# Kernel optimization log

Measured on AMD Instinct MI355X. Metric: run time of the kernel, lower is better.

The kernel has to match this reference:

```python
import jax, jax.numpy as jnp
import numpy as np

HEADS, DEPTH, KS = 4, 16, 3
PAD = KS // 2
LN_EPS = 1e-3   # keras LayerNormalization default
BN_EPS = 1e-3   # keras BatchNormalization default


def _layernorm(x, g, b):
    m = jnp.mean(x, axis=-1, keepdims=True)
    v = jnp.var(x, axis=-1, keepdims=True)
    return (x - m) * jax.lax.rsqrt(v + LN_EPS) * g + b


def setup_inputs() -> dict:
    key = jax.random.key(0)
    ks = jax.random.split(key, 12)
    B, H, W, C, FF = 4, 384, 384, 64, 128
    s = 0.05
    return {
        "x": jax.random.normal(ks[0], (B, H, W, C), jnp.float32),
        "wq": jax.random.normal(ks[1], (C, C), jnp.float32) * s,
        "wk": jax.random.normal(ks[2], (C, C), jnp.float32) * s,
        "wv": jax.random.normal(ks[3], (C, C), jnp.float32) * s,
        "ln1_g": jnp.ones((C,), jnp.float32),
        "ln1_b": jnp.zeros((C,), jnp.float32),
        "ff1_w": jax.random.normal(ks[4], (C, FF), jnp.float32) * s,
        "ff1_b": jnp.zeros((FF,), jnp.float32),
        "ff2_w": jax.random.normal(ks[5], (FF, C), jnp.float32) * s,
        "ff2_b": jnp.zeros((C,), jnp.float32),
        "ln2_g": jnp.ones((C,), jnp.float32),
        "ln2_b": jnp.zeros((C,), jnp.float32),
        "w_fuse": jax.random.normal(ks[6], (C, C), jnp.float32) * s,
        "bn_g": jax.random.uniform(ks[7], (C,), jnp.float32, 0.5, 1.5),
        "bn_b": jax.random.normal(ks[8], (C,), jnp.float32) * s,
        "bn_mean": jax.random.normal(ks[9], (C,), jnp.float32) * s,
        "bn_var": jax.random.uniform(ks[10], (C,), jnp.float32, 0.5, 1.5),
    }


def reference(x, wq, wk, wv, ln1_g, ln1_b, ff1_w, ff1_b, ff2_w, ff2_b,
              ln2_g, ln2_b, w_fuse, bn_g, bn_b, bn_mean, bn_var):
    B, H, W, C = x.shape
    # 1x1-conv projections == per-pixel dense over channels
    q = jnp.einsum('bhwc,cd->bhwd', x, wq).reshape(B, H, W, HEADS, DEPTH)
    k = jnp.einsum('bhwc,cd->bhwd', x, wk)
    v = jnp.einsum('bhwc,cd->bhwd', x, wv)
    # SAME zero-padding, matching tf.image.extract_patches
    kp = jnp.pad(k, ((0, 0), (PAD, PAD), (PAD, PAD), (0, 0)))
    vp = jnp.pad(v, ((0, 0), (PAD, PAD), (PAD, PAD), (0, 0)))
    # scores for each of the ks*ks offsets via shifted slices (no im2col blowup)
    sims = []
    for dy in range(KS):
        for dx in range(KS):
            ksh = kp[:, dy:dy + H, dx:dx + W, :].reshape(B, H, W, HEADS, DEPTH)
            sims.append(jnp.einsum('bhwnd,bhwnd->bhwn', q, ksh))
    sim = jnp.stack(sims, axis=3) / jnp.sqrt(jnp.float32(DEPTH))  # [B,H,W,ka,heads]
    attn = jax.nn.softmax(sim, axis=3)
    out = jnp.zeros_like(q)  # [B,H,W,heads,depth]
    i = 0
    for dy in range(KS):
        for dx in range(KS):
            vsh = vp[:, dy:dy + H, dx:dx + W, :].reshape(B, H, W, HEADS, DEPTH)
            out = out + attn[:, :, :, i, :, None] * vsh
            i += 1
    out = out.reshape(B, H, W, C)
    # residual (res_proj is None since C % heads == 0) + LN
    out = _layernorm(x + out, ln1_g, ln1_b)
    # token FFN with residual + LN
    ff = jax.nn.relu(jnp.einsum('bhwc,cf->bhwf', out, ff1_w) + ff1_b)
    ff = jnp.einsum('bhwf,fc->bhwc', ff, ff2_w) + ff2_b
    out = _layernorm(out + ff, ln2_g, ln2_b)
    # fuse 1x1 conv + BN (inference mode, moving stats) + relu
    out = jnp.einsum('bhwc,cd->bhwd', out, w_fuse)
    scale = bn_g * jax.lax.rsqrt(bn_var + BN_EPS)
    out = out * scale + (bn_b - bn_mean * scale)
    return jax.nn.relu(out)
```

## Files before the change

kernel.cpp:

```cpp
#include <hip/hip_runtime.h>

#define MTOT 589824

typedef __attribute__((ext_vector_type(8))) short bf16x8;
typedef __attribute__((ext_vector_type(4))) float f32x4;
#define MFMA16 __builtin_amdgcn_mfma_f32_16x16x32_bf16

__device__ __forceinline__ unsigned short f2bf(float f) {
    union { float f; unsigned u; } x; x.f = f;
    unsigned r = x.u + 0x7FFFu + ((x.u >> 16) & 1u);
    return (unsigned short)(r >> 16);
}
__device__ __forceinline__ float bf2f(unsigned short h) {
    union { unsigned u; float f; } x; x.u = ((unsigned)h) << 16;
    return x.f;
}
__device__ __forceinline__ float2 bfpair(int v) {
    union { unsigned u; float f; } a, b;
    a.u = ((unsigned)v) << 16;
    b.u = ((unsigned)v) & 0xffff0000u;
    return make_float2(a.f, b.f);
}
__device__ __forceinline__ int is_bf16(const void* ln1g) {
    return ((const unsigned short*)ln1g)[0] != 0;
}
__device__ __forceinline__ float ldp(const void* p, int i, int isbf) {
    return isbf ? bf2f(((const unsigned short*)p)[i]) : ((const float*)p)[i];
}

__global__ void k_prep(const void* wq, const void* wk, const void* wv,
                       const void* ln1g, const void* ln1b,
                       const void* ff1w, const void* ff1b,
                       const void* ff2w, const void* ff2b,
                       const void* ln2g, const void* ln2b,
                       const void* wfuse, const void* bng, const void* bnb,
                       const void* bnm, const void* bnv,
                       unsigned short* Wbase, float* P) {
    const int isbf = is_bf16(ln1g);
    const int tid = blockIdx.x * blockDim.x + threadIdx.x;
    const int stride = gridDim.x * blockDim.x;
    unsigned short* Wqkv = Wbase;
    unsigned short* W1 = Wbase + 12288;
    unsigned short* W2 = W1 + 8192;
    unsigned short* WF = W2 + 8192;
    for (int i = tid; i < 12288; i += stride) {
        int n = i >> 6, k = i & 63;
        float v;
        if (n < 64)        v = ldp(wq, k*64 + n, isbf) * 0.25f;
        else if (n < 128)  v = ldp(wk, k*64 + (n-64), isbf);
        else               v = ldp(wv, k*64 + (n-128), isbf);
        Wqkv[n*64 + k] = f2bf(v);
    }
    for (int i = tid; i < 8192; i += stride) {
        int n = i >> 6, k = i & 63;
        W1[n*64 + k] = f2bf(ldp(ff1w, k*128 + n, isbf));
    }
    for (int i = tid; i < 8192; i += stride) {
        int n = i >> 7, k = i & 127;
        W2[n*128 + k] = f2bf(ldp(ff2w, k*64 + n, isbf));
    }
    for (int i = tid; i < 4096; i += stride) {
        int n = i >> 6, k = i & 63;
        WF[n*64 + k] = f2bf(ldp(wfuse, k*64 + n, isbf));
    }
    for (int i = tid; i < 64; i += stride) {
        P[i]       = ldp(ln1g, i, isbf);
        P[64+i]    = ldp(ln1b, i, isbf);
        P[256+i]   = ldp(ff2b, i, isbf);
        P[320+i]   = ldp(ln2g, i, isbf);
        P[384+i]   = ldp(ln2b, i, isbf);
        float sc   = ldp(bng, i, isbf) * rsqrtf(ldp(bnv, i, isbf) + 1e-3f);
        P[448+i]   = sc;
        P[512+i]   = ldp(bnb, i, isbf) - ldp(bnm, i, isbf) * sc;
    }
    for (int i = tid; i < 128; i += stride) P[128+i] = ldp(ff1b, i, isbf);
}

__device__ __forceinline__ int rowOf(int hy, int hx) {
    if (hy >= 1 && hy <= 8 && hx >= 1 && hx <= 8) return (hy - 1) * 8 + (hx - 1);
    if (hy == 0) return 64 + hx;
    if (hy == 9) return 74 + hx;
    if (hx == 0) return 84 + (hy - 1);
    return 92 + (hy - 1);
}

__global__ __launch_bounds__(256) void k_fused(
    const void* __restrict__ xg, const void* __restrict__ ln1g,
    const unsigned short* __restrict__ Wqkv, const unsigned short* __restrict__ W1,
    const unsigned short* __restrict__ W2, const unsigned short* __restrict__ WF,
    const float* __restrict__ P, void* __restrict__ outg) {
    __shared__ __align__(16) unsigned short xh[112 * 64];
    __shared__ __align__(16) unsigned short kvb[112 * 132];
    __shared__ __align__(16) unsigned short qy[64 * 72];
    const int t = threadIdx.x;
    const int isbf = is_bf16(ln1g);
    const int bid = ((int)blockIdx.x & 7) * 1152 + ((int)blockIdx.x >> 3);
    const int bb = bid / 2304;
    const int tile = bid - bb * 2304;
    const int by = tile / 48, bx = tile - by * 48;
    const long imgbase = (long)bb * 147456;

    if (isbf) {
        const unsigned short* xs = (const unsigned short*)xg;
        for (int i = t; i < 800; i += 256) {
            int p = i >> 3, c8 = i & 7;
            int hy = p / 10, hx = p - hy * 10;
            int r = rowOf(hy, hx);
            int gy = by * 8 + hy - 1, gx = bx * 8 + hx - 1;
            int4 val = {0, 0, 0, 0};
            if ((unsigned)gy < 384u && (unsigned)gx < 384u)
                val = *(const int4*)(xs + (imgbase + (long)gy * 384 + gx) * 64 + c8 * 8);
            *(int4*)&xh[r * 64 + ((c8 ^ (r & 7)) << 3)] = val;
        }
    } else {
        const float* xs = (const float*)xg;
        for (int i = t; i < 1600; i += 256) {
            int p = i >> 4, c4 = i & 15;
            int hy = p / 10, hx = p - hy * 10;
            int r = rowOf(hy, hx);
            int gy = by * 8 + hy - 1, gx = bx * 8 + hx - 1;
            ushort4 hv = {0, 0, 0, 0};
            if ((unsigned)gy < 384u && (unsigned)gx < 384u) {
                float4 f = *(const float4*)(xs + (imgbase + (long)gy * 384 + gx) * 64 + c4 * 4);
                hv.x = f2bf(f.x); hv.y = f2bf(f.y); hv.z = f2bf(f.z); hv.w = f2bf(f.w);
            }
            int c8 = c4 >> 1;
            *(ushort4*)&xh[r * 64 + (((c8 ^ (r & 7)) << 3) | ((c4 & 1) << 2))] = hv;
        }
    }
    if (t < 96) {
        int4 zz = {0, 0, 0, 0};
        *(int4*)&xh[(100 + (t >> 3)) * 64 + ((t & 7) << 3)] = zz;
    }

    float4 rf0, rf1, rf2, rf3; int4 ri0, ri1;
    {
        const int px = t >> 2, qtr = t & 3;
        const long pofs = (imgbase + (long)(by*8 + (px >> 3)) * 384 + bx*8 + (px & 7)) * 64 + qtr * 16;
        if (isbf) {
            const int4* xp = (const int4*)((const unsigned short*)xg + pofs);
            ri0 = xp[0]; ri1 = xp[1];
        } else {
            const float4* xp = (const float4*)((const float*)xg + pofs);
            rf0 = xp[0]; rf1 = xp[1]; rf2 = xp[2]; rf3 = xp[3];
        }
    }
    __syncthreads();

    const int w = t >> 6, l = t & 63, lm = l & 15, q4 = l >> 4;
    #pragma unroll 2
    for (int uu = 0; uu < 14; ++uu) {
        int u = uu * 4 + w;
        int rt = u >> 3, nt = u & 7;
        int row = rt * 16 + lm, sw = row & 7;
        const bf16x8 a0 = *(const bf16x8*)&xh[row * 64 + ((q4 ^ sw) << 3)];
        const bf16x8 a1 = *(const bf16x8*)&xh[row * 64 + (((q4 + 4) ^ sw) << 3)];
        const unsigned short* wp = Wqkv + (64 + nt * 16 + lm) * 64 + q4 * 8;
        bf16x8 b0 = *(const bf16x8*)wp;
        bf16x8 b1 = *(const bf16x8*)(wp + 32);
        f32x4 acc = {0.f, 0.f, 0.f, 0.f};
        acc = MFMA16(a0, b0, acc, 0, 0, 0);
        acc = MFMA16(a1, b1, acc, 0, 0, 0);
        #pragma unroll
        for (int r = 0; r < 4; ++r)
            kvb[(rt * 16 + q4 * 4 + r) * 132 + nt * 16 + lm] = f2bf(acc[r]);
    }
    #pragma unroll
    for (int uu = 0; uu < 4; ++uu) {
        int row = uu * 16 + lm, sw = row & 7;
        const bf16x8 a0 = *(const bf16x8*)&xh[row * 64 + ((q4 ^ sw) << 3)];
        const bf16x8 a1 = *(const bf16x8*)&xh[row * 64 + (((q4 + 4) ^ sw) << 3)];
        const unsigned short* wp = Wqkv + (w * 16 + lm) * 64 + q4 * 8;
        bf16x8 b0 = *(const bf16x8*)wp;
        bf16x8 b1 = *(const bf16x8*)(wp + 32);
        f32x4 acc = {0.f, 0.f, 0.f, 0.f};
        acc = MFMA16(a0, b0, acc, 0, 0, 0);
        acc = MFMA16(a1, b1, acc, 0, 0, 0);
        #pragma unroll
        for (int r = 0; r < 4; ++r)
            qy[(uu * 16 + q4 * 4 + r) * 72 + w * 16 + lm] = f2bf(acc[r]);
    }
    __syncthreads();

    {
        const int h = w, py = l >> 3, px8 = l & 7;
        float qv[16];
        {
            const int4* qp2 = (const int4*)&qy[l * 72 + h * 16];
            int4 qa = qp2[0], qb4 = qp2[1];
            float2 p0;
            p0 = bfpair(qa.x);  qv[0]  = p0.x; qv[1]  = p0.y;
            p0 = bfpair(qa.y);  qv[2]  = p0.x; qv[3]  = p0.y;
            p0 = bfpair(qa.z);  qv[4]  = p0.x; qv[5]  = p0.y;
            p0 = bfpair(qa.w);  qv[6]  = p0.x; qv[7]  = p0.y;
            p0 = bfpair(qb4.x); qv[8]  = p0.x; qv[9]  = p0.y;
            p0 = bfpair(qb4.y); qv[10] = p0.x; qv[11] = p0.y;
            p0 = bfpair(qb4.z); qv[12] = p0.x; qv[13] = p0.y;
            p0 = bfpair(qb4.w); qv[14] = p0.x; qv[15] = p0.y;
        }
        int rn9[9];
        #pragma unroll
        for (int e = 0; e < 9; ++e) {
            int dy = e / 3, dx = e - dy * 3;
            rn9[e] = rowOf(py + dy, px8 + dx);
        }
        float w9[9];
        #pragma unroll
        for (int e = 0; e < 9; ++e) {
            const int2* kp = (const int2*)&kvb[rn9[e] * 132 + h * 16];
            float sacc = 0.f;
            #pragma unroll
            for (int j = 0; j < 4; ++j) {
                int2 kk = kp[j];
                float2 pa = bfpair(kk.x), pb = bfpair(kk.y);
                sacc += qv[j*4+0]*pa.x + qv[j*4+1]*pa.y
                      + qv[j*4+2]*pb.x + qv[j*4+3]*pb.y;
            }
            w9[e] = sacc;
        }
        float mx = w9[0];
        #pragma unroll
        for (int e = 1; e < 9; ++e) mx = fmaxf(mx, w9[e]);
        float den = 0.f;
        #pragma unroll
        for (int e = 0; e < 9; ++e) { w9[e] = __expf(w9[e] - mx); den += w9[e]; }
        const float inv = 1.f / den;
        float att[16];
        #pragma unroll
        for (int i = 0; i < 16; ++i) att[i] = 0.f;
        #pragma unroll
        for (int e = 0; e < 9; ++e) {
            const int2* vp = (const int2*)&kvb[rn9[e] * 132 + 64 + h * 16];
            const float wgt = w9[e] * inv;
            #pragma unroll
            for (int j = 0; j < 4; ++j) {
                int2 vv = vp[j];
                float2 pa = bfpair(vv.x), pb = bfpair(vv.y);
                att[j*4+0] += wgt*pa.x;
                att[j*4+1] += wgt*pa.y;
                att[j*4+2] += wgt*pb.x;
                att[j*4+3] += wgt*pb.y;
            }
        }
        int4 o0, o1;
        o0.x = (int)((unsigned)f2bf(att[0])  | ((unsigned)f2bf(att[1])  << 16));
        o0.y = (int)((unsigned)f2bf(att[2])  | ((unsigned)f2bf(att[3])  << 16));
        o0.z = (int)((unsigned)f2bf(att[4])  | ((unsigned)f2bf(att[5])  << 16));
        o0.w = (int)((unsigned)f2bf(att[6])  | ((unsigned)f2bf(att[7])  << 16));
        o1.x = (int)((unsigned)f2bf(att[8])  | ((unsigned)f2bf(att[9])  << 16));
        o1.y = (int)((unsigned)f2bf(att[10]) | ((unsigned)f2bf(att[11]) << 16));
        o1.z = (int)((unsigned)f2bf(att[12]) | ((unsigned)f2bf(att[13]) << 16));
        o1.w = (int)((unsigned)f2bf(att[14]) | ((unsigned)f2bf(att[15]) << 16));
        *(int4*)&qy[l * 72 + h * 16]     = o0;
        *(int4*)&qy[l * 72 + h * 16 + 8] = o1;
    }
    __syncthreads();

    {
        const int px = t >> 2, qtr = t & 3;
        float v[16];
        const int2* ap = (const int2*)&qy[px * 72 + qtr * 16];
        #pragma unroll
        for (int j = 0; j < 4; ++j) {
            int2 u = ap[j];
            float2 pa = bfpair(u.x), pb = bfpair(u.y);
            v[j*4+0] = pa.x; v[j*4+1] = pa.y; v[j*4+2] = pb.x; v[j*4+3] = pb.y;
        }
        if (isbf) {
            float2 pa = bfpair(ri0.x), pb = bfpair(ri0.y), pc = bfpair(ri0.z), pd = bfpair(ri0.w);
            v[0] += pa.x; v[1] += pa.y; v[2] += pb.x; v[3] += pb.y;
            v[4] += pc.x; v[5] += pc.y; v[6] += pd.x; v[7] += pd.y;
            pa = bfpair(ri1.x); pb = bfpair(ri1.y); pc = bfpair(ri1.z); pd = bfpair(ri1.w);
            v[8]  += pa.x; v[9]  += pa.y; v[10] += pb.x; v[11] += pb.y;
            v[12] += pc.x; v[13] += pc.y; v[14] += pd.x; v[15] += pd.y;
        } else {
            v[0]  += rf0.x; v[1]  += rf0.y; v[2]  += rf0.z; v[3]  += rf0.w;
            v[4]  += rf1.x; v[5]  += rf1.y; v[6]  += rf1.z; v[7]  += rf1.w;
            v[8]  += rf2.x; v[9]  += rf2.y; v[10] += rf2.z; v[11] += rf2.w;
            v[12] += rf3.x; v[13] += rf3.y; v[14] += rf3.z; v[15] += rf3.w;
        }
        float s = 0.f, ss = 0.f;
        #pragma unroll
        for (int c = 0; c < 16; ++c) { s += v[c]; ss += v[c]*v[c]; }
        s  += __shfl_xor(s, 1);  ss += __shfl_xor(ss, 1);
        s  += __shfl_xor(s, 2);  ss += __shfl_xor(ss, 2);
        const float mean = s * (1.f/64.f);
        const float var  = ss * (1.f/64.f) - mean*mean;
        const float rs   = rsqrtf(var + 1e-3f);
        unsigned short* wp2 = &qy[px * 72 + qtr * 16];
        #pragma unroll
        for (int c = 0; c < 16; ++c)
            wp2[c] = f2bf((v[c] - mean)*rs*P[qtr*16 + c] + P[64 + qtr*16 + c]);
    }
    __syncthreads();

    unsigned short* hh = kvb;
    {
        const bf16x8 a0 = *(const bf16x8*)&qy[(w*16 + lm)*72 + q4*8];
        const bf16x8 a1 = *(const bf16x8*)&qy[(w*16 + lm)*72 + 32 + q4*8];
        #pragma unroll
        for (int nt = 0; nt < 8; ++nt) {
            const unsigned short* wp = W1 + (nt*16 + lm)*64 + q4*8;
            bf16x8 b0 = *(const bf16x8*)wp;
            bf16x8 b1 = *(const bf16x8*)(wp + 32);
            f32x4 acc = {0.f, 0.f, 0.f, 0.f};
            acc = MFMA16(a0, b0, acc, 0, 0, 0);
            acc = MFMA16(a1, b1, acc, 0, 0, 0);
            const float bias = P[128 + nt*16 + lm];
            #pragma unroll
            for (int r = 0; r < 4; ++r)
                hh[(w*16 + q4*4 + r)*136 + nt*16 + lm] = f2bf(fmaxf(acc[r] + bias, 0.f));
        }
    }
    __syncthreads();
    {
        bf16x8 a[4];
        #pragma unroll
        for (int kc = 0; kc < 4; ++kc)
            a[kc] = *(const bf16x8*)&hh[(w*16 + lm)*136 + kc*32 + q4*8];
        float v2[4][4];
        #pragma unroll
        for (int nt = 0; nt < 4; ++nt) {
            f32x4 acc = {0.f, 0.f, 0.f, 0.f};
            #pragma unroll
            for (int kc = 0; kc < 4; ++kc) {
                bf16x8 b = *(const bf16x8*)(W2 + (nt*16 + lm)*128 + kc*32 + q4*8);
                acc = MFMA16(a[kc], b, acc, 0, 0, 0);
            }
            const int col = nt*16 + lm;
            const float bias = P[256 + col];
            #pragma unroll
            for (int r = 0; r < 4; ++r)
                v2[nt][r] = acc[r] + bias + bf2f(qy[(w*16 + q4*4 + r)*72 + col]);
        }
        float s[4], ss[4];
        #pragma unroll
        for (int r = 0; r < 4; ++r) {
            s[r]  = v2[0][r] + v2[1][r] + v2[2][r] + v2[3][r];
            ss[r] = v2[0][r]*v2[0][r] + v2[1][r]*v2[1][r] + v2[2][r]*v2[2][r] + v2[3][r]*v2[3][r];
        }
        #pragma unroll
        for (int mk = 1; mk <= 8; mk <<= 1) {
            #pragma unroll
            for (int r = 0; r < 4; ++r) {
                s[r]  += __shfl_xor(s[r], mk);
                ss[r] += __shfl_xor(ss[r], mk);
            }
        }
        __syncthreads();
        #pragma unroll
        for (int r = 0; r < 4; ++r) {
            const float mean = s[r] * (1.f/64.f);
            const float var  = ss[r] * (1.f/64.f) - mean*mean;
            const float rsv  = rsqrtf(var + 1e-3f);
            #pragma unroll
            for (int nt = 0; nt < 4; ++nt) {
                const int col = nt*16 + lm;
                qy[(w*16 + q4*4 + r)*72 + col] =
                    f2bf((v2[nt][r] - mean)*rsv*P[320 + col] + P[384 + col]);
            }
        }
    }
    __syncthreads();
    {
        const bf16x8 a0 = *(const bf16x8*)&qy[(w*16 + lm)*72 + q4*8];
        const bf16x8 a1 = *(const bf16x8*)&qy[(w*16 + lm)*72 + 32 + q4*8];
        float* stf = (float*)kvb + w*1024;
        unsigned short* sth = kvb + w*1024;
        #pragma unroll
        for (int nt = 0; nt < 4; ++nt) {
            const unsigned short* wp = WF + (nt*16 + lm)*64 + q4*8;
            bf16x8 b0 = *(const bf16x8*)wp;
            bf16x8 b1 = *(const bf16x8*)(wp + 32);
            f32x4 acc = {0.f, 0.f, 0.f, 0.f};
            acc = MFMA16(a0, b0, acc, 0, 0, 0);
            acc = MFMA16(a1, b1, acc, 0, 0, 0);
            const int col = nt*16 + lm;
            const float sc = P[448 + col], bi = P[512 + col];
            #pragma unroll
            for (int r = 0; r < 4; ++r) {
                float f = fmaxf(acc[r]*sc + bi, 0.f);
                if (isbf) sth[(q4*4 + r)*64 + col] = f2bf(f);
                else      stf[(q4*4 + r)*64 + col] = f;
            }
        }
    }
    __syncthreads();
    if (isbf) {
        const unsigned short* sth = kvb + w*1024;
        unsigned short* op = (unsigned short*)outg;
        #pragma unroll
        for (int i = 0; i < 2; ++i) {
            int e = (i*64 + l)*8, r = e >> 6, c = e & 63;
            int px = w*16 + r;
            long ga = (imgbase + (long)(by*8 + (px >> 3))*384 + bx*8 + (px & 7))*64 + c;
            *(int4*)(op + ga) = *(const int4*)&sth[e];
        }
    } else {
        const float* stf = (const float*)kvb + w*1024;
        float* op = (float*)outg;
        #pragma unroll
        for (int i = 0; i < 4; ++i) {
            int e = (i*64 + l)*4, r = e >> 6, c = e & 63;
            int px = w*16 + r;
            long ga = (imgbase + (long)(by*8 + (px >> 3))*384 + bx*8 + (px & 7))*64 + c;
            *(float4*)(op + ga) = *(const float4*)&stf[e];
        }
    }
}

extern "C" void kernel_launch(void* const* d_in, const int* in_sizes, int n_in,
                              void* d_out, int out_size, void* d_ws, size_t ws_size,
                              hipStream_t stream) {
    const void* x     = d_in[0];
    const void* wq    = d_in[1];
    const void* wk    = d_in[2];
    const void* wv    = d_in[3];
    const void* ln1g  = d_in[4];
    const void* ln1b  = d_in[5];
    const void* ff1w  = d_in[6];
    const void* ff1b  = d_in[7];
    const void* ff2w  = d_in[8];
    const void* ff2b  = d_in[9];
    const void* ln2g  = d_in[10];
    const void* ln2b  = d_in[11];
    const void* wfuse = d_in[12];
    const void* bng   = d_in[13];
    const void* bnb   = d_in[14];
    const void* bnm   = d_in[15];
    const void* bnv   = d_in[16];

    unsigned short* Wbase = (unsigned short*)d_ws;
    float* P = (float*)(Wbase + 32768);

    k_prep<<<64, 256, 0, stream>>>(wq, wk, wv, ln1g, ln1b, ff1w, ff1b, ff2w, ff2b,
                                   ln2g, ln2b, wfuse, bng, bnb, bnm, bnv, Wbase, P);
    k_fused<<<9216, 256, 0, stream>>>(x, ln1g, Wbase, Wbase + 12288, Wbase + 20480,
                                      Wbase + 28672, P, d_out);
}
```

Measured before the change: 603.0 us.

## Alias x halo buffer into KV shared buffer and stash early K/V tiles in registers

Removes the separate shared-memory halo buffer for x by aliasing it onto the KV buffer, cutting LDS use per block so more blocks can be resident (launch bounds now request 4 blocks per SIMD/CU). Because the first K/V tiles would overwrite halo rows still being read, their results are packed into registers and written back after an extra barrier once all projections finish. This adds register pressure, an extra __syncthreads, and more unrolled code in exchange for higher occupancy.

```diff
diff --git a/kernel.cpp b/kernel.cpp
--- a/kernel.cpp
+++ b/kernel.cpp
@@ -20,6 +20,9 @@
     a.u = ((unsigned)v) << 16;
     b.u = ((unsigned)v) & 0xffff0000u;
     return make_float2(a.f, b.f);
+}
+__device__ __forceinline__ unsigned pk2(float lo, float hi) {
+    return (unsigned)f2bf(lo) | ((unsigned)f2bf(hi) << 16);
 }
 __device__ __forceinline__ int is_bf16(const void* ln1g) {
     return ((const unsigned short*)ln1g)[0] != 0;
@@ -84,14 +87,14 @@
     return 92 + (hy - 1);
 }
 
-__global__ __launch_bounds__(256) void k_fused(
+__global__ __launch_bounds__(256, 4) void k_fused(
     const void* __restrict__ xg, const void* __restrict__ ln1g,
     const unsigned short* __restrict__ Wqkv, const unsigned short* __restrict__ W1,
     const unsigned short* __restrict__ W2, const unsigned short* __restrict__ WF,
     const float* __restrict__ P, void* __restrict__ outg) {
-    __shared__ __align__(16) unsigned short xh[112 * 64];
     __shared__ __align__(16) unsigned short kvb[112 * 132];
     __shared__ __align__(16) unsigned short qy[64 * 72];
+    unsigned short* xh = kvb;
     const int t = threadIdx.x;
     const int isbf = is_bf16(ln1g);
     const int bid = ((int)blockIdx.x & 7) * 1152 + ((int)blockIdx.x >> 3);
@@ -148,8 +151,9 @@
     __syncthreads();
 
     const int w = t >> 6, l = t & 63, lm = l & 15, q4 = l >> 4;
-    #pragma unroll 2
-    for (int uu = 0; uu < 14; ++uu) {
+    unsigned stash[16];
+    #pragma unroll
+    for (int uu = 0; uu < 8; ++uu) {
         int u = uu * 4 + w;
         int rt = u >> 3, nt = u & 7;
         int row = rt * 16 + lm, sw = row & 7;
@@ -161,9 +165,27 @@
         f32x4 acc = {0.f, 0.f, 0.f, 0.f};
         acc = MFMA16(a0, b0, acc, 0, 0, 0);
         acc = MFMA16(a1, b1, acc, 0, 0, 0);
-        #pragma unroll
-        for (int r = 0; r < 4; ++r)
-            kvb[(rt * 16 + q4 * 4 + r) * 132 + nt * 16 + lm] = f2bf(acc[r]);
+        stash[uu*2]   = pk2(acc[0], acc[1]);
+        stash[uu*2+1] = pk2(acc[2], acc[3]);
+    }
+    #pragma unroll
+    for (int uu = 0; uu < 6; ++uu) {
+        int u = 32 + uu * 4 + w;
+        int rt = u >> 3, nt = u & 7;
+        int row = rt * 16 + lm, sw = row & 7;
+        const bf16x8 a0 = *(const bf16x8*)&xh[row * 64 + ((q4 ^ sw) << 3)];
+        const bf16x8 a1 = *(const bf16x8*)&xh[row * 64 + (((q4 + 4) ^ sw) << 3)];
+        const unsigned short* wp = Wqkv + (64 + nt * 16 + lm) * 64 + q4 * 8;
+        bf16x8 b0 = *(const bf16x8*)wp;
+        bf16x8 b1 = *(const bf16x8*)(wp + 32);
+        f32x4 acc = {0.f, 0.f, 0.f, 0.f};
+        acc = MFMA16(a0, b0, acc, 0, 0, 0);
+        acc = MFMA16(a1, b1, acc, 0, 0, 0);
+        int row0 = rt * 16 + q4 * 4, col = nt * 16 + lm;
+        kvb[(row0    ) * 132 + col] = f2bf(acc[0]);
+        kvb[(row0 + 1) * 132 + col] = f2bf(acc[1]);
+        kvb[(row0 + 2) * 132 + col] = f2bf(acc[2]);
+        kvb[(row0 + 3) * 132 + col] = f2bf(acc[3]);
     }
     #pragma unroll
     for (int uu = 0; uu < 4; ++uu) {
@@ -176,9 +198,23 @@
         f32x4 acc = {0.f, 0.f, 0.f, 0.f};
         acc = MFMA16(a0, b0, acc, 0, 0, 0);
         acc = MFMA16(a1, b1, acc, 0, 0, 0);
-        #pragma unroll
-        for (int r = 0; r < 4; ++r)
-            qy[(uu * 16 + q4 * 4 + r) * 72 + w * 16 + lm] = f2bf(acc[r]);
+        int row0 = uu * 16 + q4 * 4, col = w * 16 + lm;
+        qy[(row0    ) * 72 + col] = f2bf(acc[0]);
+        qy[(row0 + 1) * 72 + col] = f2bf(acc[1]);
+        qy[(row0 + 2) * 72 + col] = f2bf(acc[2]);
+        qy[(row0 + 3) * 72 + col] = f2bf(acc[3]);
+    }
+    __syncthreads();
+    #pragma unroll
+    for (int uu = 0; uu < 8; ++uu) {
+        int u = uu * 4 + w;
+        int rt = u >> 3, nt = u & 7;
+        int row0 = rt * 16 + q4 * 4, col = nt * 16 + lm;
+        unsigned p0 = stash[uu*2], p1 = stash[uu*2+1];
+        kvb[(row0    ) * 132 + col] = (unsigned short)p0;
+        kvb[(row0 + 1) * 132 + col] = (unsigned short)(p0 >> 16);
+        kvb[(row0 + 2) * 132 + col] = (unsigned short)p1;
+        kvb[(row0 + 3) * 132 + col] = (unsigned short)(p1 >> 16);
     }
     __syncthreads();
 
@@ -243,14 +279,14 @@
             }
         }
         int4 o0, o1;
-        o0.x = (int)((unsigned)f2bf(att[0])  | ((unsigned)f2bf(att[1])  << 16));
-        o0.y = (int)((unsigned)f2bf(att[2])  | ((unsigned)f2bf(att[3])  << 16));
-        o0.z = (int)((unsigned)f2bf(att[4])  | ((unsigned)f2bf(att[5])  << 16));
-        o0.w = (int)((unsigned)f2bf(att[6])  | ((unsigned)f2bf(att[7])  << 16));
-        o1.x = (int)((unsigned)f2bf(att[8])  | ((unsigned)f2bf(att[9])  << 16));
-        o1.y = (int)((unsigned)f2bf(att[10]) | ((unsigned)f2bf(att[11]) << 16));
-        o1.z = (int)((unsigned)f2bf(att[12]) | ((unsigned)f2bf(att[13]) << 16));
-        o1.w = (int)((unsigned)f2bf(att[14]) | ((unsigned)f2bf(att[15]) << 16));
+        o0.x = (int)pk2(att[0],  att[1]);
+        o0.y = (int)pk2(att[2],  att[3]);
+        o0.z = (int)pk2(att[4],  att[5]);
+        o0.w = (int)pk2(att[6],  att[7]);
+        o1.x = (int)pk2(att[8],  att[9]);
+        o1.y = (int)pk2(att[10], att[11]);
+        o1.z = (int)pk2(att[12], att[13]);
+        o1.w = (int)pk2(att[14], att[15]);
         *(int4*)&qy[l * 72 + h * 16]     = o0;
         *(int4*)&qy[l * 72 + h * 16 + 8] = o1;
     }
```

Result: faster. 543.2 us (-9.9%).
